# Performance work log

Hardware: AMD Instinct MI355X
Metric: run time of the kernel (lower is better)

Reference implementation:

```python
import jax, jax.numpy as jnp
import numpy as np

N = 50000
E = 800000
C_IN = 64
C_OUT = 64
K = 3  # Chebyshev order (num_stacks)
LAMBDA_MAX = 2.0


def setup_inputs() -> dict:
    key = jax.random.key(0)
    ks = jax.random.split(key, 32)
    inp = {
        'X': jax.random.normal(ks[0], (N, C_IN), dtype=jnp.float32),
        'edge_index': jax.random.randint(ks[1], (2, E), 0, N, dtype=jnp.int64),
        'edge_weight': jax.random.uniform(ks[2], (E,), dtype=jnp.float32),
        'H': jax.random.normal(ks[3], (N, C_OUT), dtype=jnp.float32),
        'C': jax.random.normal(ks[4], (N, C_OUT), dtype=jnp.float32),
    }
    # 8 ChebConvs: conv_{x,h}_{i,f,c,o}; x-convs map C_IN->C_OUT, h-convs C_OUT->C_OUT
    names_x = ['Wxi', 'Wxf', 'Wxc', 'Wxo']
    names_h = ['Whi', 'Whf', 'Whc', 'Who']
    i = 5
    for nx, nh in zip(names_x, names_h):
        inp[nx] = jax.random.normal(ks[i], (K, C_IN, C_OUT), dtype=jnp.float32) * (1.0 / np.sqrt(K * C_IN)); i += 1
        inp['b' + nx[1:]] = jax.random.normal(ks[i], (C_OUT,), dtype=jnp.float32) * 0.01; i += 1
        inp[nh] = jax.random.normal(ks[i], (K, C_OUT, C_OUT), dtype=jnp.float32) * (1.0 / np.sqrt(K * C_OUT)); i += 1
        inp['b' + nh[1:]] = jax.random.normal(ks[i], (C_OUT,), dtype=jnp.float32) * 0.01; i += 1
    # per-gate biases b_i, b_f, b_c, b_o of shape [1, C_OUT] (zero-initialized in torch)
    for nm in ['bi', 'bf', 'bc', 'bo']:
        inp[nm] = jax.random.normal(ks[i], (1, C_OUT), dtype=jnp.float32) * 0.01; i += 1
    return inp


def _cheb_norm(edge_index, edge_weight, n):
    # symmetric normalization: D^-1/2 W D^-1/2 (PyG get_laplacian 'sym')
    row, col = edge_index[0], edge_index[1]
    deg = jax.ops.segment_sum(edge_weight, row, num_segments=n)
    dinv = jnp.where(deg > 0, jax.lax.rsqrt(jnp.where(deg > 0, deg, 1.0)), 0.0)
    return dinv[row] * edge_weight * dinv[col]


def _cheb_conv(x, W, b, row, col, nw, n):
    # ChebConv: out = sum_k T_k(L_hat) x @ W[k] + b, with
    # L_hat v = (2/lambda_max) * (v - A_norm v) - v
    def Lhat(v):
        agg = jax.ops.segment_sum(nw[:, None] * v[col], row, num_segments=n)
        return (2.0 / LAMBDA_MAX) * (v - agg) - v
    Tx_prev = x
    out = x @ W[0]
    k = W.shape[0]
    if k > 1:
        Tx = Lhat(x)
        out = out + Tx @ W[1]
        for j in range(2, k):
            Tx_new = 2.0 * Lhat(Tx) - Tx_prev
            out = out + Tx_new @ W[j]
            Tx_prev, Tx = Tx, Tx_new
    return out + b


def reference(X, edge_index, edge_weight, H, C,
              Wxi, bxi, Whi, bhi, Wxf, bxf, Whf, bhf,
              Wxc, bxc, Whc, bhc, Wxo, bxo, Who, bho,
              bi, bf, bc, bo):
    n = X.shape[0]
    row, col = edge_index[0], edge_index[1]
    nw = _cheb_norm(edge_index, edge_weight, n)
    cc = lambda v, W, b: _cheb_conv(v, W, b, row, col, nw, n)
    I = jax.nn.sigmoid(cc(X, Wxi, bxi) + cc(H, Whi, bhi) + bi)
    F = jax.nn.sigmoid(cc(X, Wxf, bxf) + cc(H, Whf, bhf) + bf)
    T = jnp.tanh(cc(X, Wxc, bxc) + cc(H, Whc, bhc) + bc)
    C_new = F * C + I * T
    O = jax.nn.sigmoid(cc(X, Wxo, bxo) + cc(H, Who, bho) + bo)
    H_new = O * jnp.tanh(C_new)
    return (H_new, C_new)
```

## Files before the change

### kernel.cpp

```cpp
#include <hip/hip_runtime.h>

#define N_NODES 50000
#define N_PAD   50048
#define N_EDGES 800000
#define NBE     3125
#define NB_IL   6250

typedef __attribute__((ext_vector_type(8))) short bf16x8;
typedef __attribute__((ext_vector_type(4))) float f32x4;

__device__ __forceinline__ unsigned short f2bf(float f) {
    unsigned u = __float_as_uint(f);
    u = (u + 0x7fffu + ((u >> 16) & 1u)) >> 16;
    return (unsigned short)u;
}

__device__ __forceinline__ float fsig(float x) {
    x = fminf(fmaxf(x, -30.f), 30.f);
    float t = __expf(x);
    return __fdividef(t, 1.f + t);
}
__device__ __forceinline__ float ftanh(float x) {
    x = fminf(fmaxf(x, -15.f), 15.f);
    float t = __expf(2.f * x);
    return 1.f - __fdividef(2.f, t + 1.f);
}

__device__ __forceinline__ int block_is_i32(const int* __restrict__ eiv, int t, int* sflag) {
    if (t == 0) *sflag = 0;
    __syncthreads();
    int v = eiv[1 + 2 * t];
    if (v) atomicOr(sflag, 1);
    __syncthreads();
    return *sflag;
}


__global__ __launch_bounds__(256) void k_deg_prep(
    const void* __restrict__ eiraw, const float* __restrict__ w,
    unsigned long long* __restrict__ packed, unsigned* __restrict__ rank,
    const float* __restrict__ X, const float* __restrict__ H, unsigned short* __restrict__ XH,
    const float* __restrict__ Wxi, const float* __restrict__ Whi,
    const float* __restrict__ Wxf, const float* __restrict__ Whf,
    const float* __restrict__ Wxc, const float* __restrict__ Whc,
    const float* __restrict__ Wxo, const float* __restrict__ Who,
    const float* __restrict__ bxi, const float* __restrict__ bhi,
    const float* __restrict__ bxf, const float* __restrict__ bhf,
    const float* __restrict__ bxc, const float* __restrict__ bhc,
    const float* __restrict__ bxo, const float* __restrict__ bho,
    const float* __restrict__ bgi, const float* __restrict__ bgf,
    const float* __restrict__ bgc, const float* __restrict__ bgo,
    unsigned short* __restrict__ Wf, float* __restrict__ ball) {
    __shared__ int sflag;
    int b = blockIdx.x, t = threadIdx.x;
    if (b < NBE) {
        int is32 = block_is_i32((const int*)eiraw, t, &sflag);
        int e = b * 256 + t;
        if (e >= N_EDGES) return;
        int r = is32 ? ((const int*)eiraw)[e] : (int)(((const long long*)eiraw)[e]);
        unsigned qw = (unsigned)(w[e] * 4194304.f + 0.5f);
        unsigned long long old = atomicAdd(&packed[r], (1ull << 32) | (unsigned long long)qw);
        rank[e] = (unsigned)(old >> 32);
        return;
    }
    int bb = b - NBE;
    if (bb < NB_IL) {
        int tt = bb * 256 + t;
        int node = tt >> 5, g = tt & 31;
        float4 v = (g < 16) ? *(const float4*)(X + (size_t)node * 64 + g * 4)
                            : *(const float4*)(H + (size_t)node * 64 + (g - 16) * 4);
        ushort4 o;
        o.x = f2bf(v.x); o.y = f2bf(v.y); o.z = f2bf(v.z); o.w = f2bf(v.w);
        *(ushort4*)(XH + (size_t)node * 128 + g * 4) = o;
        return;
    }
    bb -= NB_IL;
    if (bb < 48) {
        int flat = bb * 256 + t;
        int l = flat & 63, nt = (flat >> 6) & 15, ks = flat >> 10;
        int n = nt * 16 + (l & 15);
        int g = n >> 6, c = n & 63;
        const float* WX = (g == 0) ? Wxi : (g == 1) ? Wxf : (g == 2) ? Wxc : Wxo;
        const float* WH = (g == 0) ? Whi : (g == 1) ? Whf : (g == 2) ? Whc : Who;
        int k0 = ks * 32 + (l >> 4) * 8;
        unsigned short ov[8];
#pragma unroll
        for (int j = 0; j < 8; j++) {
            int k = k0 + j;
            int bsel = k >> 7, ch = k & 127;
            const float* W = (ch < 64) ? WX : WH;
            int kk = ch & 63;
            float v;
            if (bsel == 0)      v = W[kk * 64 + c] - W[2 * 4096 + kk * 64 + c];
            else if (bsel == 1) v = -W[4096 + kk * 64 + c];
            else                v = 2.f * W[2 * 4096 + kk * 64 + c];
            ov[j] = f2bf(v);
        }
        uint4 o;
        o.x = (unsigned)ov[0] | ((unsigned)ov[1] << 16);
        o.y = (unsigned)ov[2] | ((unsigned)ov[3] << 16);
        o.z = (unsigned)ov[4] | ((unsigned)ov[5] << 16);
        o.w = (unsigned)ov[6] | ((unsigned)ov[7] << 16);
        *(uint4*)(Wf + (size_t)flat * 8) = o;
    } else {
        int g = t >> 6, c = t & 63;
        const float* BX = (g == 0) ? bxi : (g == 1) ? bxf : (g == 2) ? bxc : bxo;
        const float* BH = (g == 0) ? bhi : (g == 1) ? bhf : (g == 2) ? bhc : bho;
        const float* BG = (g == 0) ? bgi : (g == 1) ? bgf : (g == 2) ? bgc : bgo;
        ball[t] = BX[c] + BH[c] + BG[c];
    }
}


__global__ __launch_bounds__(256) void k_scan1(const unsigned long long* __restrict__ packed,
                                               int* __restrict__ rp, int* __restrict__ part,
                                               float* __restrict__ dinv) {
    __shared__ int s[256];
    int t = threadIdx.x, i = blockIdx.x * 256 + t;
    unsigned long long p = (i < N_NODES) ? packed[i] : 0ull;
    int v = (int)(p >> 32);
    s[t] = v; __syncthreads();
    for (int d = 1; d < 256; d <<= 1) {
        int add = (t >= d) ? s[t - d] : 0;
        __syncthreads();
        s[t] += add;
        __syncthreads();
    }
    if (i < N_NODES) {
        rp[i] = s[t] - v;
        float dg = (float)(unsigned)(p & 0xffffffffu) * (1.f / 4194304.f);
        dinv[i] = (dg > 0.f) ? rsqrtf(dg) : 0.f;
        if (i == N_NODES - 1) rp[N_NODES] = s[t];
    }
    if (t == 255) part[blockIdx.x] = s[255];
}

__global__ __launch_bounds__(256) void k_scan2(int* __restrict__ part, int nb) {
    __shared__ int s[256];
    int t = threadIdx.x;
    int v = (t < nb) ? part[t] : 0;
    s[t] = v; __syncthreads();
    for (int d = 1; d < 256; d <<= 1) {
        int add = (t >= d) ? s[t - d] : 0;
        __syncthreads();
        s[t] += add;
        __syncthreads();
    }
    if (t < nb) part[t] = s[t] - v;
}

__global__ __launch_bounds__(256) void k_scatter(const void* __restrict__ eiraw, const float* __restrict__ w,
                                                 const unsigned* __restrict__ rank,
                                                 const float* __restrict__ dinv, const int* __restrict__ rp,
                                                 const int* __restrict__ part,
                                                 int* __restrict__ colp, float* __restrict__ nwp) {
    __shared__ int sflag;
    int t = threadIdx.x;
    int is32 = block_is_i32((const int*)eiraw, t, &sflag);
    int e = blockIdx.x * 256 + t;
    if (e >= N_EDGES) return;
    int r, c;
    if (is32) { r = ((const int*)eiraw)[e]; c = ((const int*)eiraw)[N_EDGES + e]; }
    else      { r = (int)(((const long long*)eiraw)[e]); c = (int)(((const long long*)eiraw)[N_EDGES + e]); }
    int pos = rp[r] + part[r >> 8] + (int)rank[e];
    colp[pos] = c;
    nwp[pos] = dinv[r] * w[e] * dinv[c];
}


__global__ __launch_bounds__(256) void k_spmv_bf(const unsigned short* __restrict__ src,
                                                 unsigned short* __restrict__ dst,
                                                 const int* __restrict__ rp, const int* __restrict__ part,
                                                 const int* __restrict__ colp, const float* __restrict__ nwp) {
    int wid = threadIdx.x >> 6, lane = threadIdx.x & 63;
    int node = blockIdx.x * 4 + wid;
    if (node >= N_NODES) return;
    int s = rp[node] + part[node >> 8];
    int e = rp[node + 1] + part[(node + 1) >> 8];
    float a0 = 0.f, a1 = 0.f;
    for (int jb = s; jb < e; jb += 8) {
        int   c[8]; float wv[8]; unsigned vv[8];
#pragma unroll
        for (int k = 0; k < 8; k++) {
            int j = jb + k;
            int jc = (j < e) ? j : (e - 1);
            c[k]  = colp[jc];
            wv[k] = (j < e) ? nwp[jc] : 0.f;
        }
#pragma unroll
        for (int k = 0; k < 8; k++)
            vv[k] = *(const unsigned*)(src + (size_t)c[k] * 128 + lane * 2);
#pragma unroll
        for (int k = 0; k < 8; k++) {
            a0 = fmaf(wv[k], __uint_as_float(vv[k] << 16), a0);
            a1 = fmaf(wv[k], __uint_as_float(vv[k] & 0xffff0000u), a1);
        }
    }
    unsigned o = (unsigned)f2bf(a0) | ((unsigned)f2bf(a1) << 16);
    *(unsigned*)(dst + (size_t)node * 128 + lane * 2) = o;
}


__global__ __launch_bounds__(256) void k_gemm_mfma(
    const unsigned short* __restrict__ XH, const unsigned short* __restrict__ U1,
    const unsigned short* __restrict__ U2, const unsigned short* __restrict__ Wf,
    const float* __restrict__ ball, const float* __restrict__ C, float* __restrict__ out) {
    __shared__ __align__(16) uint4 Bs[2][1024];

    int t = threadIdx.x;
    int wid = t >> 6, lane = t & 63;
    int col = lane & 15, quad = lane >> 4;
    int m0 = blockIdx.x * 64 + wid * 16;
    int arow = m0 + col;

    f32x4 acc[16];
#pragma unroll
    for (int i = 0; i < 16; i++) acc[i] = (f32x4){0.f, 0.f, 0.f, 0.f};

    const unsigned short* srcs[3] = {XH, U1, U2};

    bf16x8 a_cur = *(const bf16x8*)(srcs[0] + (size_t)arow * 128 + quad * 8);
    const uint4* g0 = (const uint4*)Wf;
    uint4 p0 = g0[t], p1 = g0[t + 256], p2 = g0[t + 512], p3 = g0[t + 768];

    for (int ks = 0; ks < 12; ks++) {
        uint4* dstb = Bs[ks & 1];
        dstb[t] = p0; dstb[t + 256] = p1; dstb[t + 512] = p2; dstb[t + 768] = p3;
        __syncthreads();
        bf16x8 a_nxt = a_cur;
        if (ks < 11) {
            int ks1 = ks + 1;
            const uint4* g = (const uint4*)(Wf + (size_t)ks1 * 8192);
            p0 = g[t]; p1 = g[t + 256]; p2 = g[t + 512]; p3 = g[t + 768];
            a_nxt = *(const bf16x8*)(srcs[ks1 >> 2] + (size_t)arow * 128 + (ks1 & 3) * 32 + quad * 8);
        }
        const unsigned short* B = (const unsigned short*)Bs[ks & 1];
#pragma unroll
        for (int nt = 0; nt < 16; nt++) {
            bf16x8 bfrag = *(const bf16x8*)(B + nt * 512 + lane * 8);
            acc[nt] = __builtin_amdgcn_mfma_f32_16x16x32_bf16(a_cur, bfrag, acc[nt], 0, 0, 0);
        }
        a_cur = a_nxt;
    }

    float bI[4], bF[4], bT[4], bO[4];
#pragma unroll
    for (int cq = 0; cq < 4; cq++) {
        int c = cq * 16 + col;
        bI[cq] = ball[c]; bF[cq] = ball[64 + c]; bT[cq] = ball[128 + c]; bO[cq] = ball[192 + c];
    }
#pragma unroll
    for (int r = 0; r < 4; r++) {
        int node = m0 + quad * 4 + r;
        if (node >= N_NODES) continue;
#pragma unroll
        for (int cq = 0; cq < 4; cq++) {
            int c = cq * 16 + col;
            float ig = fsig(acc[0 + cq][r]  + bI[cq]);
            float fg = fsig(acc[4 + cq][r]  + bF[cq]);
            float tg = ftanh(acc[8 + cq][r] + bT[cq]);
            float og = fsig(acc[12 + cq][r] + bO[cq]);
            float cv = fmaf(fg, C[(size_t)node * 64 + c], ig * tg);
            out[(size_t)node * 64 + c] = og * ftanh(cv);
            out[(size_t)N_NODES * 64 + (size_t)node * 64 + c] = cv;
        }
    }
}


extern "C" void kernel_launch(void* const* d_in, const int* in_sizes, int n_in,
                              void* d_out, int out_size, void* d_ws, size_t ws_size,
                              hipStream_t stream) {
    const float* X   = (const float*)d_in[0];
    const void*  ei  = d_in[1];
    const float* w   = (const float*)d_in[2];
    const float* H   = (const float*)d_in[3];
    const float* C   = (const float*)d_in[4];
    const float* Wxi = (const float*)d_in[5];  const float* bxi = (const float*)d_in[6];
    const float* Whi = (const float*)d_in[7];  const float* bhi = (const float*)d_in[8];
    const float* Wxf = (const float*)d_in[9];  const float* bxf = (const float*)d_in[10];
    const float* Whf = (const float*)d_in[11]; const float* bhf = (const float*)d_in[12];
    const float* Wxc = (const float*)d_in[13]; const float* bxc = (const float*)d_in[14];
    const float* Whc = (const float*)d_in[15]; const float* bhc = (const float*)d_in[16];
    const float* Wxo = (const float*)d_in[17]; const float* bxo = (const float*)d_in[18];
    const float* Who = (const float*)d_in[19]; const float* bho = (const float*)d_in[20];
    const float* bgi = (const float*)d_in[21]; const float* bgf = (const float*)d_in[22];
    const float* bgc = (const float*)d_in[23]; const float* bgo = (const float*)d_in[24];
    float* out = (float*)d_out;

    char* ws = (char*)d_ws;
    size_t off = 0;
    auto alloc = [&](size_t bytes) -> char* {
        char* p = ws + off;
        off = (off + bytes + 255) & ~(size_t)255;
        return p;
    };
    unsigned long long* packed = (unsigned long long*)alloc((size_t)N_NODES * 8);
    unsigned* rank = (unsigned*)alloc((size_t)N_EDGES * 4);
    int*   rp   = (int*)alloc((N_NODES + 1) * 4);
    int*   part = (int*)alloc(256 * 4);
    float* dinv = (float*)alloc(N_NODES * 4);
    int*   colp = (int*)alloc((size_t)(N_EDGES + 8) * 4);
    float* nwp  = (float*)alloc((size_t)(N_EDGES + 8) * 4);
    unsigned short* XH = (unsigned short*)alloc((size_t)N_PAD * 128 * 2);
    unsigned short* U1 = (unsigned short*)alloc((size_t)N_PAD * 128 * 2);
    unsigned short* U2 = (unsigned short*)alloc((size_t)N_PAD * 128 * 2);
    unsigned short* Wf = (unsigned short*)alloc((size_t)12 * 16 * 64 * 8 * 2);
    float* ball = (float*)alloc(256 * 4);
    (void)ws_size; (void)in_sizes; (void)n_in; (void)out_size;

    hipMemsetAsync(packed, 0, (size_t)N_NODES * 8, stream);

    int nbN = (N_NODES + 255) / 256;

    k_deg_prep<<<NBE + NB_IL + 49, 256, 0, stream>>>(ei, w, packed, rank, X, H, XH,
                                                     Wxi, Whi, Wxf, Whf, Wxc, Whc, Wxo, Who,
                                                     bxi, bhi, bxf, bhf, bxc, bhc, bxo, bho,
                                                     bgi, bgf, bgc, bgo, Wf, ball);
    k_scan1<<<nbN, 256, 0, stream>>>(packed, rp, part, dinv);
    k_scan2<<<1, 256, 0, stream>>>(part, nbN);
    k_scatter<<<NBE, 256, 0, stream>>>(ei, w, rank, dinv, rp, part, colp, nwp);
    k_spmv_bf<<<(N_NODES + 3) / 4, 256, 0, stream>>>(XH, U1, rp, part, colp, nwp);
    k_spmv_bf<<<(N_NODES + 3) / 4, 256, 0, stream>>>(U1, U2, rp, part, colp, nwp);
    k_gemm_mfma<<<(N_NODES + 63) / 64, 256, 0, stream>>>(XH, U1, U2, Wf, ball, C, out);
}
```

Baseline: 294.9 us.

## Replicate degree counters per XCD and use workgroup-scope atomics for CSR build

After: 299.6 us. No clear change (+1.6%).

```diff
diff --git a/kernel.cpp b/kernel.cpp
--- a/kernel.cpp
+++ b/kernel.cpp
@@ -24,6 +24,12 @@
     x = fminf(fmaxf(x, -15.f), 15.f);
     float t = __expf(2.f * x);
     return 1.f - __fdividef(2.f, t + 1.f);
+}
+
+__device__ __forceinline__ unsigned xcd_id() {
+    unsigned x;
+    asm volatile("s_getreg_b32 %0, hwreg(HW_REG_XCC_ID)" : "=s"(x));
+    return x & 7;
 }
 
 __device__ __forceinline__ int block_is_i32(const int* __restrict__ eiv, int t, int* sflag) {
@@ -38,7 +44,7 @@
 
 __global__ __launch_bounds__(256) void k_deg_prep(
     const void* __restrict__ eiraw, const float* __restrict__ w,
-    unsigned long long* __restrict__ packed, unsigned* __restrict__ rank,
+    unsigned long long* __restrict__ packed8, unsigned short* __restrict__ rank,
     const float* __restrict__ X, const float* __restrict__ H, unsigned short* __restrict__ XH,
     const float* __restrict__ Wxi, const float* __restrict__ Whi,
     const float* __restrict__ Wxf, const float* __restrict__ Whf,
@@ -58,9 +64,12 @@
         int e = b * 256 + t;
         if (e >= N_EDGES) return;
         int r = is32 ? ((const int*)eiraw)[e] : (int)(((const long long*)eiraw)[e]);
+        unsigned rep = xcd_id();
         unsigned qw = (unsigned)(w[e] * 4194304.f + 0.5f);
-        unsigned long long old = atomicAdd(&packed[r], (1ull << 32) | (unsigned long long)qw);
-        rank[e] = (unsigned)(old >> 32);
+        unsigned long long old = __hip_atomic_fetch_add(
+            &packed8[(size_t)rep * N_NODES + r], (1ull << 32) | (unsigned long long)qw,
+            __ATOMIC_RELAXED, __HIP_MEMORY_SCOPE_WORKGROUP);
+        rank[e] = (unsigned short)(((old >> 32) & 255u) | (rep << 8));
         return;
     }
     int bb = b - NBE;
@@ -112,14 +121,24 @@
 }
 
 
-__global__ __launch_bounds__(256) void k_scan1(const unsigned long long* __restrict__ packed,
+__global__ __launch_bounds__(256) void k_scan1(const unsigned long long* __restrict__ packed8,
                                                int* __restrict__ rp, int* __restrict__ part,
-                                               float* __restrict__ dinv) {
+                                               float* __restrict__ dinv,
+                                               unsigned long long* __restrict__ baserep) {
     __shared__ int s[256];
     int t = threadIdx.x, i = blockIdx.x * 256 + t;
-    unsigned long long p = (i < N_NODES) ? packed[i] : 0ull;
-    int v = (int)(p >> 32);
-    s[t] = v; __syncthreads();
+    int cnt = 0;
+    unsigned long long baseq = 0, sumw = 0;
+    if (i < N_NODES) {
+#pragma unroll
+        for (int r = 0; r < 8; r++) {
+            unsigned long long p = packed8[(size_t)r * N_NODES + i];
+            baseq |= ((unsigned long long)(cnt & 255)) << (8 * r);
+            cnt += (int)(p >> 32);
+            sumw += (p & 0xffffffffull);
+        }
+    }
+    s[t] = cnt; __syncthreads();
     for (int d = 1; d < 256; d <<= 1) {
         int add = (t >= d) ? s[t - d] : 0;
         __syncthreads();
@@ -127,8 +146,9 @@
         __syncthreads();
     }
     if (i < N_NODES) {
-        rp[i] = s[t] - v;
-        float dg = (float)(unsigned)(p & 0xffffffffu) * (1.f / 4194304.f);
+        rp[i] = s[t] - cnt;
+        baserep[i] = baseq;
+        float dg = (float)sumw * (1.f / 4194304.f);
         dinv[i] = (dg > 0.f) ? rsqrtf(dg) : 0.f;
         if (i == N_NODES - 1) rp[N_NODES] = s[t];
     }
@@ -150,9 +170,10 @@
 }
 
 __global__ __launch_bounds__(256) void k_scatter(const void* __restrict__ eiraw, const float* __restrict__ w,
-                                                 const unsigned* __restrict__ rank,
+                                                 const unsigned short* __restrict__ rank,
                                                  const float* __restrict__ dinv, const int* __restrict__ rp,
                                                  const int* __restrict__ part,
+                                                 const unsigned long long* __restrict__ baserep,
                                                  int* __restrict__ colp, float* __restrict__ nwp) {
     __shared__ int sflag;
     int t = threadIdx.x;
@@ -162,7 +183,10 @@
     int r, c;
     if (is32) { r = ((const int*)eiraw)[e]; c = ((const int*)eiraw)[N_EDGES + e]; }
     else      { r = (int)(((const long long*)eiraw)[e]); c = (int)(((const long long*)eiraw)[N_EDGES + e]); }
-    int pos = rp[r] + part[r >> 8] + (int)rank[e];
+    unsigned rr = rank[e];
+    int rep = rr >> 8, rk = rr & 255;
+    int base = (int)((baserep[r] >> (8 * rep)) & 255u);
+    int pos = rp[r] + part[r >> 8] + base + rk;
     colp[pos] = c;
     nwp[pos] = dinv[r] * w[e] * dinv[c];
 }
@@ -295,8 +319,9 @@
         off = (off + bytes + 255) & ~(size_t)255;
         return p;
     };
-    unsigned long long* packed = (unsigned long long*)alloc((size_t)N_NODES * 8);
-    unsigned* rank = (unsigned*)alloc((size_t)N_EDGES * 4);
+    unsigned long long* packed8 = (unsigned long long*)alloc((size_t)8 * N_NODES * 8);
+    unsigned long long* baserep = (unsigned long long*)alloc((size_t)N_NODES * 8);
+    unsigned short* rank = (unsigned short*)alloc((size_t)N_EDGES * 2);
     int*   rp   = (int*)alloc((N_NODES + 1) * 4);
     int*   part = (int*)alloc(256 * 4);
     float* dinv = (float*)alloc(N_NODES * 4);
@@ -309,17 +334,17 @@
     float* ball = (float*)alloc(256 * 4);
     (void)ws_size; (void)in_sizes; (void)n_in; (void)out_size;
 
-    hipMemsetAsync(packed, 0, (size_t)N_NODES * 8, stream);
+    hipMemsetAsync(packed8, 0, (size_t)8 * N_NODES * 8, stream);
 
     int nbN = (N_NODES + 255) / 256;
 
-    k_deg_prep<<<NBE + NB_IL + 49, 256, 0, stream>>>(ei, w, packed, rank, X, H, XH,
+    k_deg_prep<<<NBE + NB_IL + 49, 256, 0, stream>>>(ei, w, packed8, rank, X, H, XH,
                                                      Wxi, Whi, Wxf, Whf, Wxc, Whc, Wxo, Who,
                                                      bxi, bhi, bxf, bhf, bxc, bhc, bxo, bho,
                                                      bgi, bgf, bgc, bgo, Wf, ball);
-    k_scan1<<<nbN, 256, 0, stream>>>(packed, rp, part, dinv);
+    k_scan1<<<nbN, 256, 0, stream>>>(packed8, rp, part, dinv, baserep);
     k_scan2<<<1, 256, 0, stream>>>(part, nbN);
-    k_scatter<<<NBE, 256, 0, stream>>>(ei, w, rank, dinv, rp, part, colp, nwp);
+    k_scatter<<<NBE, 256, 0, stream>>>(ei, w, rank, dinv, rp, part, baserep, colp, nwp);
     k_spmv_bf<<<(N_NODES + 3) / 4, 256, 0, stream>>>(XH, U1, rp, part, colp, nwp);
     k_spmv_bf<<<(N_NODES + 3) / 4, 256, 0, stream>>>(U1, U2, rp, part, colp, nwp);
     k_gemm_mfma<<<(N_NODES + 63) / 64, 256, 0, stream>>>(XH, U1, U2, Wf, ball, C, out);
```

## Fuse all graph-conv LSTM stages into one cooperative persistent kernel with grid syncs

Applied to the files above, without the earlier changes.

After: 780.6 us. 2.65x slower.

```diff
diff --git a/kernel.cpp b/kernel.cpp
--- a/kernel.cpp
+++ b/kernel.cpp
@@ -1,10 +1,15 @@
 #include <hip/hip_runtime.h>
+#include <hip/hip_cooperative_groups.h>
+
+namespace cg = cooperative_groups;
 
 #define N_NODES 50000
 #define N_PAD   50048
 #define N_EDGES 800000
 #define NBE     3125
 #define NB_IL   6250
+#define NGRP    196
+#define NTILE   782
 
 typedef __attribute__((ext_vector_type(8))) short bf16x8;
 typedef __attribute__((ext_vector_type(4))) float f32x4;
@@ -14,7 +19,6 @@
     u = (u + 0x7fffu + ((u >> 16) & 1u)) >> 16;
     return (unsigned short)u;
 }
-
 __device__ __forceinline__ float fsig(float x) {
     x = fminf(fmaxf(x, -30.f), 30.f);
     float t = __expf(x);
@@ -26,243 +30,240 @@
     return 1.f - __fdividef(2.f, t + 1.f);
 }
 
-__device__ __forceinline__ int block_is_i32(const int* __restrict__ eiv, int t, int* sflag) {
-    if (t == 0) *sflag = 0;
-    __syncthreads();
-    int v = eiv[1 + 2 * t];
-    if (v) atomicOr(sflag, 1);
-    __syncthreads();
-    return *sflag;
-}
-
-
-__global__ __launch_bounds__(256) void k_deg_prep(
-    const void* __restrict__ eiraw, const float* __restrict__ w,
-    unsigned long long* __restrict__ packed, unsigned* __restrict__ rank,
-    const float* __restrict__ X, const float* __restrict__ H, unsigned short* __restrict__ XH,
-    const float* __restrict__ Wxi, const float* __restrict__ Whi,
-    const float* __restrict__ Wxf, const float* __restrict__ Whf,
-    const float* __restrict__ Wxc, const float* __restrict__ Whc,
-    const float* __restrict__ Wxo, const float* __restrict__ Who,
-    const float* __restrict__ bxi, const float* __restrict__ bhi,
-    const float* __restrict__ bxf, const float* __restrict__ bhf,
-    const float* __restrict__ bxc, const float* __restrict__ bhc,
-    const float* __restrict__ bxo, const float* __restrict__ bho,
-    const float* __restrict__ bgi, const float* __restrict__ bgf,
-    const float* __restrict__ bgc, const float* __restrict__ bgo,
-    unsigned short* __restrict__ Wf, float* __restrict__ ball) {
-    __shared__ int sflag;
-    int b = blockIdx.x, t = threadIdx.x;
-    if (b < NBE) {
-        int is32 = block_is_i32((const int*)eiraw, t, &sflag);
-        int e = b * 256 + t;
-        if (e >= N_EDGES) return;
-        int r = is32 ? ((const int*)eiraw)[e] : (int)(((const long long*)eiraw)[e]);
-        unsigned qw = (unsigned)(w[e] * 4194304.f + 0.5f);
-        unsigned long long old = atomicAdd(&packed[r], (1ull << 32) | (unsigned long long)qw);
-        rank[e] = (unsigned)(old >> 32);
-        return;
-    }
-    int bb = b - NBE;
-    if (bb < NB_IL) {
-        int tt = bb * 256 + t;
-        int node = tt >> 5, g = tt & 31;
-        float4 v = (g < 16) ? *(const float4*)(X + (size_t)node * 64 + g * 4)
-                            : *(const float4*)(H + (size_t)node * 64 + (g - 16) * 4);
-        ushort4 o;
-        o.x = f2bf(v.x); o.y = f2bf(v.y); o.z = f2bf(v.z); o.w = f2bf(v.w);
-        *(ushort4*)(XH + (size_t)node * 128 + g * 4) = o;
-        return;
-    }
-    bb -= NB_IL;
-    if (bb < 48) {
-        int flat = bb * 256 + t;
-        int l = flat & 63, nt = (flat >> 6) & 15, ks = flat >> 10;
-        int n = nt * 16 + (l & 15);
-        int g = n >> 6, c = n & 63;
-        const float* WX = (g == 0) ? Wxi : (g == 1) ? Wxf : (g == 2) ? Wxc : Wxo;
-        const float* WH = (g == 0) ? Whi : (g == 1) ? Whf : (g == 2) ? Whc : Who;
-        int k0 = ks * 32 + (l >> 4) * 8;
-        unsigned short ov[8];
-#pragma unroll
-        for (int j = 0; j < 8; j++) {
-            int k = k0 + j;
-            int bsel = k >> 7, ch = k & 127;
-            const float* W = (ch < 64) ? WX : WH;
-            int kk = ch & 63;
-            float v;
-            if (bsel == 0)      v = W[kk * 64 + c] - W[2 * 4096 + kk * 64 + c];
-            else if (bsel == 1) v = -W[4096 + kk * 64 + c];
-            else                v = 2.f * W[2 * 4096 + kk * 64 + c];
-            ov[j] = f2bf(v);
-        }
-        uint4 o;
-        o.x = (unsigned)ov[0] | ((unsigned)ov[1] << 16);
-        o.y = (unsigned)ov[2] | ((unsigned)ov[3] << 16);
-        o.z = (unsigned)ov[4] | ((unsigned)ov[5] << 16);
-        o.w = (unsigned)ov[6] | ((unsigned)ov[7] << 16);
-        *(uint4*)(Wf + (size_t)flat * 8) = o;
-    } else {
-        int g = t >> 6, c = t & 63;
-        const float* BX = (g == 0) ? bxi : (g == 1) ? bxf : (g == 2) ? bxc : bxo;
-        const float* BH = (g == 0) ? bhi : (g == 1) ? bhf : (g == 2) ? bhc : bho;
-        const float* BG = (g == 0) ? bgi : (g == 1) ? bgf : (g == 2) ? bgc : bgo;
-        ball[t] = BX[c] + BH[c] + BG[c];
-    }
-}
-
-
-__global__ __launch_bounds__(256) void k_scan1(const unsigned long long* __restrict__ packed,
-                                               int* __restrict__ rp, int* __restrict__ part,
-                                               float* __restrict__ dinv) {
+struct KArgs {
+    const void* ei; const float* w;
+    const float* X; const float* H; const float* C;
+    const float* Wxi; const float* Whi; const float* Wxf; const float* Whf;
+    const float* Wxc; const float* Whc; const float* Wxo; const float* Who;
+    const float* bxi; const float* bhi; const float* bxf; const float* bhf;
+    const float* bxc; const float* bhc; const float* bxo; const float* bho;
+    const float* bgi; const float* bgf; const float* bgc; const float* bgo;
+    float* out;
+    unsigned long long* packed; unsigned char* rank;
+    int* rp; int* part; float* dinv; int* flag;
+    int* colp; float* nwp;
+    unsigned short* XH; unsigned short* U1; unsigned short* U2;
+    unsigned short* Wf; float* ball;
+};
+
+__device__ __forceinline__ void spmv_phase(const unsigned short* __restrict__ src,
+                                           unsigned short* __restrict__ dst,
+                                           const int* __restrict__ rp, const int* psum,
+                                           const int* __restrict__ colp,
+                                           const float* __restrict__ nwp, int nb) {
+    int wid = threadIdx.x >> 6, lane = threadIdx.x & 63;
+    for (int node = blockIdx.x * 4 + wid; node < N_NODES; node += nb * 4) {
+        int s = rp[node] + psum[node >> 8];
+        int e = rp[node + 1] + psum[(node + 1) >> 8];
+        float a0 = 0.f, a1 = 0.f;
+        for (int jb = s; jb < e; jb += 16) {
+            int c[16]; float wv[16]; unsigned vv[16];
+#pragma unroll
+            for (int k = 0; k < 16; k++) {
+                int j = jb + k;
+                int jc = (j < e) ? j : (e - 1);
+                c[k]  = colp[jc];
+                wv[k] = (j < e) ? nwp[jc] : 0.f;
+            }
+#pragma unroll
+            for (int k = 0; k < 16; k++)
+                vv[k] = *(const unsigned*)(src + (size_t)c[k] * 128 + lane * 2);
+#pragma unroll
+            for (int k = 0; k < 16; k++) {
+                a0 = fmaf(wv[k], __uint_as_float(vv[k] << 16), a0);
+                a1 = fmaf(wv[k], __uint_as_float(vv[k] & 0xffff0000u), a1);
+            }
+        }
+        unsigned o = (unsigned)f2bf(a0) | ((unsigned)f2bf(a1) << 16);
+        *(unsigned*)(dst + (size_t)node * 128 + lane * 2) = o;
+    }
+}
+
+__global__ __launch_bounds__(256, 4) void k_mega(KArgs a) {
     __shared__ int s[256];
-    int t = threadIdx.x, i = blockIdx.x * 256 + t;
-    unsigned long long p = (i < N_NODES) ? packed[i] : 0ull;
-    int v = (int)(p >> 32);
-    s[t] = v; __syncthreads();
-    for (int d = 1; d < 256; d <<= 1) {
-        int add = (t >= d) ? s[t - d] : 0;
+    __shared__ int psum[256];
+    __shared__ __align__(16) uint4 Bs[2][1024];
+
+    cg::grid_group grid = cg::this_grid();
+    int t = threadIdx.x;
+    int nb = gridDim.x;
+
+    for (int i = blockIdx.x * 256 + t; i < N_NODES; i += nb * 256) a.packed[i] = 0ull;
+    if (blockIdx.x == 0) {
+        int v = 0;
+        for (int i = 1 + 2 * t; i < 8192; i += 512) v |= ((const int*)a.ei)[i];
+        s[t] = v; __syncthreads();
+        if (t == 0) {
+            int acc = 0;
+            for (int k = 0; k < 256; k++) acc |= s[k];
+            *a.flag = acc ? 1 : 0;
+        }
+    }
+    grid.sync();
+    int is32 = *a.flag;
+
+    for (int vb = blockIdx.x; vb < NBE + NB_IL + 49; vb += nb) {
+        if (vb < NBE) {
+            int e = vb * 256 + t;
+            if (e < N_EDGES) {
+                int r = is32 ? ((const int*)a.ei)[e] : (int)(((const long long*)a.ei)[e]);
+                unsigned qw = (unsigned)(a.w[e] * 4194304.f + 0.5f);
+                unsigned long long old = atomicAdd(&a.packed[r], (1ull << 32) | (unsigned long long)qw);
+                a.rank[e] = (unsigned char)(old >> 32);
+            }
+        } else if (vb < NBE + NB_IL) {
+            int tt = (vb - NBE) * 256 + t;
+            int node = tt >> 5, g = tt & 31;
+            float4 v = (g < 16) ? *(const float4*)(a.X + (size_t)node * 64 + g * 4)
+                                : *(const float4*)(a.H + (size_t)node * 64 + (g - 16) * 4);
+            ushort4 o;
+            o.x = f2bf(v.x); o.y = f2bf(v.y); o.z = f2bf(v.z); o.w = f2bf(v.w);
+            *(ushort4*)(a.XH + (size_t)node * 128 + g * 4) = o;
+        } else if (vb < NBE + NB_IL + 48) {
+            int flat = (vb - NBE - NB_IL) * 256 + t;
+            int l = flat & 63, nt = (flat >> 6) & 15, ks = flat >> 10;
+            int n = nt * 16 + (l & 15);
+            int g = n >> 6, c = n & 63;
+            const float* WX = (g == 0) ? a.Wxi : (g == 1) ? a.Wxf : (g == 2) ? a.Wxc : a.Wxo;
+            const float* WH = (g == 0) ? a.Whi : (g == 1) ? a.Whf : (g == 2) ? a.Whc : a.Who;
+            int k0 = ks * 32 + (l >> 4) * 8;
+            unsigned short ov[8];
+#pragma unroll
+            for (int j = 0; j < 8; j++) {
+                int k = k0 + j;
+                int bsel = k >> 7, ch = k & 127;
+                const float* W = (ch < 64) ? WX : WH;
+                int kk = ch & 63;
+                float v;
+                if (bsel == 0)      v = W[kk * 64 + c] - W[2 * 4096 + kk * 64 + c];
+                else if (bsel == 1) v = -W[4096 + kk * 64 + c];
+                else                v = 2.f * W[2 * 4096 + kk * 64 + c];
+                ov[j] = f2bf(v);
+            }
+            uint4 o;
+            o.x = (unsigned)ov[0] | ((unsigned)ov[1] << 16);
+            o.y = (unsigned)ov[2] | ((unsigned)ov[3] << 16);
+            o.z = (unsigned)ov[4] | ((unsigned)ov[5] << 16);
+            o.w = (unsigned)ov[6] | ((unsigned)ov[7] << 16);
+            *(uint4*)(a.Wf + (size_t)flat * 8) = o;
+        } else {
+            int g = t >> 6, c = t & 63;
+            const float* BX = (g == 0) ? a.bxi : (g == 1) ? a.bxf : (g == 2) ? a.bxc : a.bxo;
+            const float* BH = (g == 0) ? a.bhi : (g == 1) ? a.bhf : (g == 2) ? a.bhc : a.bho;
+            const float* BG = (g == 0) ? a.bgi : (g == 1) ? a.bgf : (g == 2) ? a.bgc : a.bgo;
+            a.ball[t] = BX[c] + BH[c] + BG[c];
+        }
+    }
+    grid.sync();
+
+    for (int vb = blockIdx.x; vb < NGRP; vb += nb) {
+        int i = vb * 256 + t;
+        unsigned long long p = (i < N_NODES) ? a.packed[i] : 0ull;
+        int v = (int)(p >> 32);
+        s[t] = v; __syncthreads();
+        for (int d = 1; d < 256; d <<= 1) {
+            int add = (t >= d) ? s[t - d] : 0;
+            __syncthreads();
+            s[t] += add;
+            __syncthreads();
+        }
+        if (i < N_NODES) {
+            a.rp[i] = s[t] - v;
+            float dg = (float)(unsigned)(p & 0xffffffffu) * (1.f / 4194304.f);
+            a.dinv[i] = (dg > 0.f) ? rsqrtf(dg) : 0.f;
+            if (i == N_NODES - 1) a.rp[N_NODES] = s[t];
+        }
+        if (t == 255) a.part[vb] = s[255];
+    }
+    grid.sync();
+
+    {
+        int v = (t < NGRP) ? a.part[t] : 0;
+        s[t] = v; __syncthreads();
+        for (int d = 1; d < 256; d <<= 1) {
+            int add = (t >= d) ? s[t - d] : 0;
+            __syncthreads();
+            s[t] += add;
+            __syncthreads();
+        }
+        psum[t] = s[t] - v;
         __syncthreads();
-        s[t] += add;
-        __syncthreads();
-    }
-    if (i < N_NODES) {
-        rp[i] = s[t] - v;
-        float dg = (float)(unsigned)(p & 0xffffffffu) * (1.f / 4194304.f);
-        dinv[i] = (dg > 0.f) ? rsqrtf(dg) : 0.f;
-        if (i == N_NODES - 1) rp[N_NODES] = s[t];
-    }
-    if (t == 255) part[blockIdx.x] = s[255];
-}
-
-__global__ __launch_bounds__(256) void k_scan2(int* __restrict__ part, int nb) {
-    __shared__ int s[256];
-    int t = threadIdx.x;
-    int v = (t < nb) ? part[t] : 0;
-    s[t] = v; __syncthreads();
-    for (int d = 1; d < 256; d <<= 1) {
-        int add = (t >= d) ? s[t - d] : 0;
-        __syncthreads();
-        s[t] += add;
-        __syncthreads();
-    }
-    if (t < nb) part[t] = s[t] - v;
-}
-
-__global__ __launch_bounds__(256) void k_scatter(const void* __restrict__ eiraw, const float* __restrict__ w,
-                                                 const unsigned* __restrict__ rank,
-                                                 const float* __restrict__ dinv, const int* __restrict__ rp,
-                                                 const int* __restrict__ part,
-                                                 int* __restrict__ colp, float* __restrict__ nwp) {
-    __shared__ int sflag;
-    int t = threadIdx.x;
-    int is32 = block_is_i32((const int*)eiraw, t, &sflag);
-    int e = blockIdx.x * 256 + t;
-    if (e >= N_EDGES) return;
-    int r, c;
-    if (is32) { r = ((const int*)eiraw)[e]; c = ((const int*)eiraw)[N_EDGES + e]; }
-    else      { r = (int)(((const long long*)eiraw)[e]); c = (int)(((const long long*)eiraw)[N_EDGES + e]); }
-    int pos = rp[r] + part[r >> 8] + (int)rank[e];
-    colp[pos] = c;
-    nwp[pos] = dinv[r] * w[e] * dinv[c];
-}
-
-
-__global__ __launch_bounds__(256) void k_spmv_bf(const unsigned short* __restrict__ src,
-                                                 unsigned short* __restrict__ dst,
-                                                 const int* __restrict__ rp, const int* __restrict__ part,
-                                                 const int* __restrict__ colp, const float* __restrict__ nwp) {
-    int wid = threadIdx.x >> 6, lane = threadIdx.x & 63;
-    int node = blockIdx.x * 4 + wid;
-    if (node >= N_NODES) return;
-    int s = rp[node] + part[node >> 8];
-    int e = rp[node + 1] + part[(node + 1) >> 8];
-    float a0 = 0.f, a1 = 0.f;
-    for (int jb = s; jb < e; jb += 8) {
-        int   c[8]; float wv[8]; unsigned vv[8];
-#pragma unroll
-        for (int k = 0; k < 8; k++) {
-            int j = jb + k;
-            int jc = (j < e) ? j : (e - 1);
-            c[k]  = colp[jc];
-            wv[k] = (j < e) ? nwp[jc] : 0.f;
-        }
-#pragma unroll
-        for (int k = 0; k < 8; k++)
-            vv[k] = *(const unsigned*)(src + (size_t)c[k] * 128 + lane * 2);
-#pragma unroll
-        for (int k = 0; k < 8; k++) {
-            a0 = fmaf(wv[k], __uint_as_float(vv[k] << 16), a0);
-            a1 = fmaf(wv[k], __uint_as_float(vv[k] & 0xffff0000u), a1);
-        }
-    }
-    unsigned o = (unsigned)f2bf(a0) | ((unsigned)f2bf(a1) << 16);
-    *(unsigned*)(dst + (size_t)node * 128 + lane * 2) = o;
-}
-
-
-__global__ __launch_bounds__(256) void k_gemm_mfma(
-    const unsigned short* __restrict__ XH, const unsigned short* __restrict__ U1,
-    const unsigned short* __restrict__ U2, const unsigned short* __restrict__ Wf,
-    const float* __restrict__ ball, const float* __restrict__ C, float* __restrict__ out) {
-    __shared__ __align__(16) uint4 Bs[2][1024];
-
-    int t = threadIdx.x;
-    int wid = t >> 6, lane = t & 63;
-    int col = lane & 15, quad = lane >> 4;
-    int m0 = blockIdx.x * 64 + wid * 16;
-    int arow = m0 + col;
-
-    f32x4 acc[16];
-#pragma unroll
-    for (int i = 0; i < 16; i++) acc[i] = (f32x4){0.f, 0.f, 0.f, 0.f};
-
-    const unsigned short* srcs[3] = {XH, U1, U2};
-
-    bf16x8 a_cur = *(const bf16x8*)(srcs[0] + (size_t)arow * 128 + quad * 8);
-    const uint4* g0 = (const uint4*)Wf;
-    uint4 p0 = g0[t], p1 = g0[t + 256], p2 = g0[t + 512], p3 = g0[t + 768];
-
-    for (int ks = 0; ks < 12; ks++) {
-        uint4* dstb = Bs[ks & 1];
-        dstb[t] = p0; dstb[t + 256] = p1; dstb[t + 512] = p2; dstb[t + 768] = p3;
-        __syncthreads();
-        bf16x8 a_nxt = a_cur;
-        if (ks < 11) {
-            int ks1 = ks + 1;
-            const uint4* g = (const uint4*)(Wf + (size_t)ks1 * 8192);
-            p0 = g[t]; p1 = g[t + 256]; p2 = g[t + 512]; p3 = g[t + 768];
-            a_nxt = *(const bf16x8*)(srcs[ks1 >> 2] + (size_t)arow * 128 + (ks1 & 3) * 32 + quad * 8);
-        }
-        const unsigned short* B = (const unsigned short*)Bs[ks & 1];
-#pragma unroll
-        for (int nt = 0; nt < 16; nt++) {
-            bf16x8 bfrag = *(const bf16x8*)(B + nt * 512 + lane * 8);
-            acc[nt] = __builtin_amdgcn_mfma_f32_16x16x32_bf16(a_cur, bfrag, acc[nt], 0, 0, 0);
-        }
-        a_cur = a_nxt;
-    }
-
-    float bI[4], bF[4], bT[4], bO[4];
-#pragma unroll
-    for (int cq = 0; cq < 4; cq++) {
-        int c = cq * 16 + col;
-        bI[cq] = ball[c]; bF[cq] = ball[64 + c]; bT[cq] = ball[128 + c]; bO[cq] = ball[192 + c];
-    }
-#pragma unroll
-    for (int r = 0; r < 4; r++) {
-        int node = m0 + quad * 4 + r;
-        if (node >= N_NODES) continue;
-#pragma unroll
-        for (int cq = 0; cq < 4; cq++) {
-            int c = cq * 16 + col;
-            float ig = fsig(acc[0 + cq][r]  + bI[cq]);
-            float fg = fsig(acc[4 + cq][r]  + bF[cq]);
-            float tg = ftanh(acc[8 + cq][r] + bT[cq]);
-            float og = fsig(acc[12 + cq][r] + bO[cq]);
-            float cv = fmaf(fg, C[(size_t)node * 64 + c], ig * tg);
-            out[(size_t)node * 64 + c] = og * ftanh(cv);
-            out[(size_t)N_NODES * 64 + (size_t)node * 64 + c] = cv;
+    }
+    for (int e = blockIdx.x * 256 + t; e < N_EDGES; e += nb * 256) {
+        int r, c;
+        if (is32) { r = ((const int*)a.ei)[e]; c = ((const int*)a.ei)[N_EDGES + e]; }
+        else      { r = (int)(((const long long*)a.ei)[e]); c = (int)(((const long long*)a.ei)[N_EDGES + e]); }
+        int pos = a.rp[r] + psum[r >> 8] + (int)a.rank[e];
+        a.colp[pos] = c;
+        a.nwp[pos] = a.dinv[r] * a.w[e] * a.dinv[c];
+    }
+    grid.sync();
+
+    spmv_phase(a.XH, a.U1, a.rp, psum, a.colp, a.nwp, nb);
+    grid.sync();
+    spmv_phase(a.U1, a.U2, a.rp, psum, a.colp, a.nwp, nb);
+    grid.sync();
+
+    {
+        int wid = t >> 6, lane = t & 63;
+        int col = lane & 15, quad = lane >> 4;
+        const unsigned short* srcs[3] = {a.XH, a.U1, a.U2};
+        for (int tile = blockIdx.x; tile < NTILE; tile += nb) {
+            int m0 = tile * 64 + wid * 16;
+            int arow = m0 + col;
+
+            f32x4 acc[16];
+#pragma unroll
+            for (int i = 0; i < 16; i++) acc[i] = (f32x4){0.f, 0.f, 0.f, 0.f};
+
+            bf16x8 a_cur = *(const bf16x8*)(srcs[0] + (size_t)arow * 128 + quad * 8);
+            const uint4* g0 = (const uint4*)a.Wf;
+            uint4 p0 = g0[t], p1 = g0[t + 256], p2 = g0[t + 512], p3 = g0[t + 768];
+
+            for (int ks = 0; ks < 12; ks++) {
+                uint4* dstb = Bs[ks & 1];
+                dstb[t] = p0; dstb[t + 256] = p1; dstb[t + 512] = p2; dstb[t + 768] = p3;
+                __syncthreads();
+                bf16x8 a_nxt = a_cur;
+                if (ks < 11) {
+                    int ks1 = ks + 1;
+                    const uint4* g = (const uint4*)(a.Wf + (size_t)ks1 * 8192);
+                    p0 = g[t]; p1 = g[t + 256]; p2 = g[t + 512]; p3 = g[t + 768];
+                    a_nxt = *(const bf16x8*)(srcs[ks1 >> 2] + (size_t)arow * 128 + (ks1 & 3) * 32 + quad * 8);
+                }
+                const unsigned short* B = (const unsigned short*)Bs[ks & 1];
+#pragma unroll
+                for (int nt = 0; nt < 16; nt++) {
+                    bf16x8 bfrag = *(const bf16x8*)(B + nt * 512 + lane * 8);
+                    acc[nt] = __builtin_amdgcn_mfma_f32_16x16x32_bf16(a_cur, bfrag, acc[nt], 0, 0, 0);
+                }
+                a_cur = a_nxt;
+            }
+
+            float bI[4], bF[4], bT[4], bO[4];
+#pragma unroll
+            for (int cq = 0; cq < 4; cq++) {
+                int c = cq * 16 + col;
+                bI[cq] = a.ball[c]; bF[cq] = a.ball[64 + c];
+                bT[cq] = a.ball[128 + c]; bO[cq] = a.ball[192 + c];
+            }
+#pragma unroll
+            for (int r = 0; r < 4; r++) {
+                int node = m0 + quad * 4 + r;
+                if (node >= N_NODES) continue;
+#pragma unroll
+                for (int cq = 0; cq < 4; cq++) {
+                    int c = cq * 16 + col;
+                    float ig = fsig(acc[0 + cq][r]  + bI[cq]);
+                    float fg = fsig(acc[4 + cq][r]  + bF[cq]);
+                    float tg = ftanh(acc[8 + cq][r] + bT[cq]);
+                    float og = fsig(acc[12 + cq][r] + bO[cq]);
+                    float cv = fmaf(fg, a.C[(size_t)node * 64 + c], ig * tg);
+                    a.out[(size_t)node * 64 + c] = og * ftanh(cv);
+                    a.out[(size_t)N_NODES * 64 + (size_t)node * 64 + c] = cv;
+                }
+            }
+            __syncthreads();
         }
     }
 }
@@ -271,23 +272,6 @@
 extern "C" void kernel_launch(void* const* d_in, const int* in_sizes, int n_in,
                               void* d_out, int out_size, void* d_ws, size_t ws_size,
                               hipStream_t stream) {
-    const float* X   = (const float*)d_in[0];
-    const void*  ei  = d_in[1];
-    const float* w   = (const float*)d_in[2];
-    const float* H   = (const float*)d_in[3];
-    const float* C   = (const float*)d_in[4];
-    const float* Wxi = (const float*)d_in[5];  const float* bxi = (const float*)d_in[6];
-    const float* Whi = (const float*)d_in[7];  const float* bhi = (const float*)d_in[8];
-    const float* Wxf = (const float*)d_in[9];  const float* bxf = (const float*)d_in[10];
-    const float* Whf = (const float*)d_in[11]; const float* bhf = (const float*)d_in[12];
-    const float* Wxc = (const float*)d_in[13]; const float* bxc = (const float*)d_in[14];
-    const float* Whc = (const float*)d_in[15]; const float* bhc = (const float*)d_in[16];
-    const float* Wxo = (const float*)d_in[17]; const float* bxo = (const float*)d_in[18];
-    const float* Who = (const float*)d_in[19]; const float* bho = (const float*)d_in[20];
-    const float* bgi = (const float*)d_in[21]; const float* bgf = (const float*)d_in[22];
-    const float* bgc = (const float*)d_in[23]; const float* bgo = (const float*)d_in[24];
-    float* out = (float*)d_out;
-
     char* ws = (char*)d_ws;
     size_t off = 0;
     auto alloc = [&](size_t bytes) -> char* {
@@ -295,32 +279,46 @@
         off = (off + bytes + 255) & ~(size_t)255;
         return p;
     };
-    unsigned long long* packed = (unsigned long long*)alloc((size_t)N_NODES * 8);
-    unsigned* rank = (unsigned*)alloc((size_t)N_EDGES * 4);
-    int*   rp   = (int*)alloc((N_NODES + 1) * 4);
-    int*   part = (int*)alloc(256 * 4);
-    float* dinv = (float*)alloc(N_NODES * 4);
-    int*   colp = (int*)alloc((size_t)(N_EDGES + 8) * 4);
-    float* nwp  = (float*)alloc((size_t)(N_EDGES + 8) * 4);
-    unsigned short* XH = (unsigned short*)alloc((size_t)N_PAD * 128 * 2);
-    unsigned short* U1 = (unsigned short*)alloc((size_t)N_PAD * 128 * 2);
-    unsigned short* U2 = (unsigned short*)alloc((size_t)N_PAD * 128 * 2);
-    unsigned short* Wf = (unsigned short*)alloc((size_t)12 * 16 * 64 * 8 * 2);
-    float* ball = (float*)alloc(256 * 4);
+
+    KArgs ka;
+    ka.X   = (const float*)d_in[0];
+    ka.ei  = d_in[1];
+    ka.w   = (const float*)d_in[2];
+    ka.H   = (const float*)d_in[3];
+    ka.C   = (const float*)d_in[4];
+    ka.Wxi = (const float*)d_in[5];  ka.bxi = (const float*)d_in[6];
+    ka.Whi = (const float*)d_in[7];  ka.bhi = (const float*)d_in[8];
+    ka.Wxf = (const float*)d_in[9];  ka.bxf = (const float*)d_in[10];
+    ka.Whf = (const float*)d_in[11]; ka.bhf = (const float*)d_in[12];
+    ka.Wxc = (const float*)d_in[13]; ka.bxc = (const float*)d_in[14];
+    ka.Whc = (const float*)d_in[15]; ka.bhc = (const float*)d_in[16];
+    ka.Wxo = (const float*)d_in[17]; ka.bxo = (const float*)d_in[18];
+    ka.Who = (const float*)d_in[19]; ka.bho = (const float*)d_in[20];
+    ka.bgi = (const float*)d_in[21]; ka.bgf = (const float*)d_in[22];
+    ka.bgc = (const float*)d_in[23]; ka.bgo = (const float*)d_in[24];
+    ka.out = (float*)d_out;
+
+    ka.packed = (unsigned long long*)alloc((size_t)N_NODES * 8);
+    ka.rank   = (unsigned char*)alloc((size_t)N_EDGES);
+    ka.rp     = (int*)alloc((N_NODES + 1) * 4);
+    ka.part   = (int*)alloc(256 * 4);
+    ka.dinv   = (float*)alloc(N_NODES * 4);
+    ka.flag   = (int*)alloc(4);
+    ka.colp   = (int*)alloc((size_t)(N_EDGES + 16) * 4);
+    ka.nwp    = (float*)alloc((size_t)(N_EDGES + 16) * 4);
+    ka.XH     = (unsigned short*)alloc((size_t)N_PAD * 128 * 2);
+    ka.U1     = (unsigned short*)alloc((size_t)N_PAD * 128 * 2);
+    ka.U2     = (unsigned short*)alloc((size_t)N_PAD * 128 * 2);
+    ka.Wf     = (unsigned short*)alloc((size_t)12 * 16 * 64 * 8 * 2);
+    ka.ball   = (float*)alloc(256 * 4);
     (void)ws_size; (void)in_sizes; (void)n_in; (void)out_size;
 
-    hipMemsetAsync(packed, 0, (size_t)N_NODES * 8, stream);
-
-    int nbN = (N_NODES + 255) / 256;
-
-    k_deg_prep<<<NBE + NB_IL + 49, 256, 0, stream>>>(ei, w, packed, rank, X, H, XH,
-                                                     Wxi, Whi, Wxf, Whf, Wxc, Whc, Wxo, Who,
-                                                     bxi, bhi, bxf, bhf, bxc, bhc, bxo, bho,
-                                                     bgi, bgf, bgc, bgo, Wf, ball);
-    k_scan1<<<nbN, 256, 0, stream>>>(packed, rp, part, dinv);
-    k_scan2<<<1, 256, 0, stream>>>(part, nbN);
-    k_scatter<<<NBE, 256, 0, stream>>>(ei, w, rank, dinv, rp, part, colp, nwp);
-    k_spmv_bf<<<(N_NODES + 3) / 4, 256, 0, stream>>>(XH, U1, rp, part, colp, nwp);
-    k_spmv_bf<<<(N_NODES + 3) / 4, 256, 0, stream>>>(U1, U2, rp, part, colp, nwp);
-    k_gemm_mfma<<<(N_NODES + 63) / 64, 256, 0, stream>>>(XH, U1, U2, Wf, ball, C, out);
-}
+    int bpc = 0;
+    hipOccupancyMaxActiveBlocksPerMultiprocessor(&bpc, k_mega, 256, 0);
+    int nblk = bpc * 256;
+    if (nblk < 256)  nblk = 256;
+    if (nblk > 1024) nblk = 1024;
+
+    void* params[] = { (void*)&ka };
+    hipLaunchCooperativeKernel((void*)k_mega, dim3(nblk), dim3(256), params, 0, stream);
+}
```
